# Performance work log

Measured on AMD Instinct MI355X. Metric: run time of the kernel, lower is better.

Reference implementation:

```python
import jax, jax.numpy as jnp
import numpy as np

IN_FEATURES = 8192
OUT_FEATURES = 8192
NNZ = 671088  # in*out*(1-0.99)
BATCH = 1024


def setup_inputs() -> dict:
    key = jax.random.key(0)
    kx, kv, kr, kc = jax.random.split(key, 4)
    x = jax.random.normal(kx, (BATCH, IN_FEATURES), dtype=jnp.float32)
    # values initialized ~ N(0,1) / sqrt(in_features), matching the module
    values = jax.random.normal(kv, (NNZ,), dtype=jnp.float32) * (1.0 / np.sqrt(IN_FEATURES))
    bias = jnp.zeros((OUT_FEATURES,), dtype=jnp.float32)
    rows = jax.random.randint(kr, (NNZ,), 0, IN_FEATURES, dtype=jnp.int32)
    cols = jax.random.randint(kc, (NNZ,), 0, OUT_FEATURES, dtype=jnp.int32)
    return {"x": x, "values": values, "bias": bias, "rows": rows, "cols": cols}


def reference(x, values, bias, rows, cols):
    # Materialize the sparse (in, out) weight via scatter-add.
    # Duplicate (row, col) pairs sum, matching torch COO .coalesce().
    W = jnp.zeros((IN_FEATURES, OUT_FEATURES), dtype=values.dtype)
    W = W.at[rows, cols].add(values)
    # res = addmm(bias, x, W) == x @ W + bias
    return x @ W + bias[None, :]
```

## Files before the change

### kernel.cpp

```cpp
#include <hip/hip_runtime.h>
#include <stdint.h>

#define IN_F   8192
#define OUT_F  8192
#define BATCH  1024
#define BT     8
#define NBT    (BATCH / BT)
#define MAIN_THREADS 1024
#define GROUPS_PER_WAVE 4
#define L_PREF 160
#define XTILE_BYTES (IN_F * 16)
#define CSTRIDE 16

#if __has_builtin(__builtin_amdgcn_fdot2) && __has_builtin(__builtin_amdgcn_perm)
#define USE_DOT2 1
typedef _Float16 half2v __attribute__((ext_vector_type(2)));
#else
#define USE_DOT2 0
#endif

typedef float f32x2 __attribute__((ext_vector_type(2)));


__device__ __forceinline__ unsigned f32_to_bf16_bits_rne(float f) {
    union { float f; unsigned u; } v; v.f = f;
    unsigned u = v.u;
    unsigned r = u + 0x7FFFu + ((u >> 16) & 1u);
    return r >> 16;
}
__device__ __forceinline__ float bf16_hi_bits_to_f32(unsigned b) {
    union { unsigned u; float f; } v; v.u = b & 0xFFFF0000u; return v.f;
}
__device__ __forceinline__ f32x2 unpack_pair(unsigned u) {
    union { unsigned u; float f; } lo, hi;
    lo.u = u << 16; hi.u = u & 0xFFFF0000u;
    f32x2 r; r.x = lo.f; r.y = hi.f; return r;
}

#if USE_DOT2
__device__ __forceinline__ unsigned val_bits(float f) {
    return (unsigned)__builtin_bit_cast(unsigned short, (_Float16)f);
}
__device__ __forceinline__ unsigned x_bits(float f) {
    return (unsigned)__builtin_bit_cast(unsigned short, (_Float16)f);
}
#else
__device__ __forceinline__ unsigned val_bits(float f) { return f32_to_bf16_bits_rne(f); }
__device__ __forceinline__ unsigned x_bits(float f)   { return f32_to_bf16_bits_rne(f); }
#endif

__global__ void scatter_kernel(const int* __restrict__ rows, const int* __restrict__ cols,
                               const float* __restrict__ vals,
                               int* __restrict__ counts, unsigned* __restrict__ ell,
                               int nnz, int L) {
    int t = blockIdx.x * blockDim.x + threadIdx.x;
    int i0 = t * 4;
    if (i0 + 3 < nnz) {
        int4   r4 = *(const int4*)(rows + i0);
        int4   c4 = *(const int4*)(cols + i0);
        float4 v4 = *(const float4*)(vals + i0);
        int c0 = c4.x, c1 = c4.y, c2 = c4.z, c3 = c4.w;
        unsigned pk0 = (val_bits(v4.x) << 16) | ((unsigned)r4.x << 3);
        unsigned pk1 = (val_bits(v4.y) << 16) | ((unsigned)r4.y << 3);
        unsigned pk2 = (val_bits(v4.z) << 16) | ((unsigned)r4.z << 3);
        unsigned pk3 = (val_bits(v4.w) << 16) | ((unsigned)r4.w << 3);
        int s0 = atomicAdd(&counts[c0 * CSTRIDE], 1);
        int s1 = atomicAdd(&counts[c1 * CSTRIDE], 1);
        int s2 = atomicAdd(&counts[c2 * CSTRIDE], 1);
        int s3 = atomicAdd(&counts[c3 * CSTRIDE], 1);
        if (s0 < L) ell[(size_t)(c0 >> 6) * (L * 64) + ((s0 >> 2) << 8) + ((c0 & 63) << 2) + (s0 & 3)] = pk0;
        if (s1 < L) ell[(size_t)(c1 >> 6) * (L * 64) + ((s1 >> 2) << 8) + ((c1 & 63) << 2) + (s1 & 3)] = pk1;
        if (s2 < L) ell[(size_t)(c2 >> 6) * (L * 64) + ((s2 >> 2) << 8) + ((c2 & 63) << 2) + (s2 & 3)] = pk2;
        if (s3 < L) ell[(size_t)(c3 >> 6) * (L * 64) + ((s3 >> 2) << 8) + ((c3 & 63) << 2) + (s3 & 3)] = pk3;
    } else {
        for (int i = i0; i < nnz; ++i) {
            int c = cols[i];
            unsigned pk = (val_bits(vals[i]) << 16) | ((unsigned)rows[i] << 3);
            int s = atomicAdd(&counts[c * CSTRIDE], 1);
            if (s < L)
                ell[(size_t)(c >> 6) * (L * 64) + ((s >> 2) << 8) + ((c & 63) << 2) + (s & 3)] = pk;
        }
    }
}

#if USE_DOT2
__device__ __forceinline__ void process_pair8(unsigned pk0, unsigned pk1, const char* xbase,
        float& a0, float& a1, float& a2, float& a3,
        float& a4, float& a5, float& a6, float& a7) {
    unsigned off0 = pk0 & 0xFFF8u;
    unsigned off1 = pk1 & 0xFFF8u;
    uint4 q0 = *(const uint4*)(xbase + off0 * 2);
    uint4 q1 = *(const uint4*)(xbase + off1 * 2);
    unsigned vv = __builtin_amdgcn_perm(pk1, pk0, 0x07060302u);
    half2v vh = __builtin_bit_cast(half2v, vv);
    unsigned e0 = __builtin_amdgcn_perm(q1.x, q0.x, 0x05040100u);
    unsigned o0 = __builtin_amdgcn_perm(q1.x, q0.x, 0x07060302u);
    unsigned e1 = __builtin_amdgcn_perm(q1.y, q0.y, 0x05040100u);
    unsigned o1 = __builtin_amdgcn_perm(q1.y, q0.y, 0x07060302u);
    unsigned e2 = __builtin_amdgcn_perm(q1.z, q0.z, 0x05040100u);
    unsigned o2 = __builtin_amdgcn_perm(q1.z, q0.z, 0x07060302u);
    unsigned e3 = __builtin_amdgcn_perm(q1.w, q0.w, 0x05040100u);
    unsigned o3 = __builtin_amdgcn_perm(q1.w, q0.w, 0x07060302u);
    a0 = __builtin_amdgcn_fdot2(__builtin_bit_cast(half2v, e0), vh, a0, false);
    a1 = __builtin_amdgcn_fdot2(__builtin_bit_cast(half2v, o0), vh, a1, false);
    a2 = __builtin_amdgcn_fdot2(__builtin_bit_cast(half2v, e1), vh, a2, false);
    a3 = __builtin_amdgcn_fdot2(__builtin_bit_cast(half2v, o1), vh, a3, false);
    a4 = __builtin_amdgcn_fdot2(__builtin_bit_cast(half2v, e2), vh, a4, false);
    a5 = __builtin_amdgcn_fdot2(__builtin_bit_cast(half2v, o2), vh, a5, false);
    a6 = __builtin_amdgcn_fdot2(__builtin_bit_cast(half2v, e3), vh, a6, false);
    a7 = __builtin_amdgcn_fdot2(__builtin_bit_cast(half2v, o3), vh, a7, false);
}
#else
__device__ __forceinline__ void process_entry8(unsigned pk, const char* xbase,
                                               f32x2& a01, f32x2& a23, f32x2& a45, f32x2& a67) {
    float val = bf16_hi_bits_to_f32(pk);
    f32x2 vv; vv.x = val; vv.y = val;
    unsigned off = pk & 0xFFF8u;
    uint4 d = *(const uint4*)(xbase + off * 2);
    a01 = __builtin_elementwise_fma(unpack_pair(d.x), vv, a01);
    a23 = __builtin_elementwise_fma(unpack_pair(d.y), vv, a23);
    a45 = __builtin_elementwise_fma(unpack_pair(d.z), vv, a45);
    a67 = __builtin_elementwise_fma(unpack_pair(d.w), vv, a67);
}
#endif

__global__ __launch_bounds__(MAIN_THREADS) void spmm_kernel(
        const float* __restrict__ x,
        const float* __restrict__ bias,
        const int* __restrict__ counts,
        const unsigned* __restrict__ ell,
        float* __restrict__ out, int L) {
    extern __shared__ uint4 xl[];
    int w = blockIdx.x;
    int bt = w >> 1;
    int half = w & 1;
    int t = threadIdx.x;
    int b0 = bt * BT;

    for (int r = t; r < IN_F; r += MAIN_THREADS) {
        unsigned u0 = x_bits(x[(b0 + 0) * IN_F + r]);
        unsigned u1 = x_bits(x[(b0 + 1) * IN_F + r]);
        unsigned u2 = x_bits(x[(b0 + 2) * IN_F + r]);
        unsigned u3 = x_bits(x[(b0 + 3) * IN_F + r]);
        unsigned u4 = x_bits(x[(b0 + 4) * IN_F + r]);
        unsigned u5 = x_bits(x[(b0 + 5) * IN_F + r]);
        unsigned u6 = x_bits(x[(b0 + 6) * IN_F + r]);
        unsigned u7 = x_bits(x[(b0 + 7) * IN_F + r]);
        uint4 d;
        d.x = (u1 << 16) | u0;
        d.y = (u3 << 16) | u2;
        d.z = (u5 << 16) | u4;
        d.w = (u7 << 16) | u6;
        xl[r] = d;
    }
    __syncthreads();

    const char* xbase = (const char*)xl;
    int wave = t >> 6;
    int lane = t & 63;
    int n4cap = L >> 2;

#pragma unroll 1
    for (int it = 0; it < GROUPS_PER_WAVE; ++it) {
        int g = half * 64 + wave * GROUPS_PER_WAVE + it;
        int col = (g << 6) + lane;
        int cnt = counts[col * CSTRIDE];
#pragma unroll
        for (int off = 32; off; off >>= 1) cnt = max(cnt, __shfl_xor(cnt, off, 64));
        int n4 = (cnt + 3) >> 2;
        n4 = min(n4, n4cap);
        const uint4* ep = (const uint4*)(ell + (size_t)g * (L * 64));
        float bv = bias[col];
#if USE_DOT2
        float a0 = 0.f, a1 = 0.f, a2 = 0.f, a3 = 0.f;
        float a4 = 0.f, a5 = 0.f, a6 = 0.f, a7 = 0.f;
        if (n4 > 0) {
            uint4 q = ep[lane];
#pragma unroll 1
            for (int s4 = 1; s4 < n4; ++s4) {
                uint4 qn = ep[s4 * 64 + lane];
                process_pair8(q.x, q.y, xbase, a0, a1, a2, a3, a4, a5, a6, a7);
                process_pair8(q.z, q.w, xbase, a0, a1, a2, a3, a4, a5, a6, a7);
                q = qn;
            }
            process_pair8(q.x, q.y, xbase, a0, a1, a2, a3, a4, a5, a6, a7);
            process_pair8(q.z, q.w, xbase, a0, a1, a2, a3, a4, a5, a6, a7);
        }
        out[(size_t)(b0 + 0) * OUT_F + col] = a0 + bv;
        out[(size_t)(b0 + 1) * OUT_F + col] = a1 + bv;
        out[(size_t)(b0 + 2) * OUT_F + col] = a2 + bv;
        out[(size_t)(b0 + 3) * OUT_F + col] = a3 + bv;
        out[(size_t)(b0 + 4) * OUT_F + col] = a4 + bv;
        out[(size_t)(b0 + 5) * OUT_F + col] = a5 + bv;
        out[(size_t)(b0 + 6) * OUT_F + col] = a6 + bv;
        out[(size_t)(b0 + 7) * OUT_F + col] = a7 + bv;
#else
        f32x2 a01 = {0.f, 0.f}, a23 = {0.f, 0.f}, a45 = {0.f, 0.f}, a67 = {0.f, 0.f};
        if (n4 > 0) {
            uint4 q = ep[lane];
#pragma unroll 1
            for (int s4 = 1; s4 < n4; ++s4) {
                uint4 qn = ep[s4 * 64 + lane];
                process_entry8(q.x, xbase, a01, a23, a45, a67);
                process_entry8(q.y, xbase, a01, a23, a45, a67);
                process_entry8(q.z, xbase, a01, a23, a45, a67);
                process_entry8(q.w, xbase, a01, a23, a45, a67);
                q = qn;
            }
            process_entry8(q.x, xbase, a01, a23, a45, a67);
            process_entry8(q.y, xbase, a01, a23, a45, a67);
            process_entry8(q.z, xbase, a01, a23, a45, a67);
            process_entry8(q.w, xbase, a01, a23, a45, a67);
        }
        out[(size_t)(b0 + 0) * OUT_F + col] = a01.x + bv;
        out[(size_t)(b0 + 1) * OUT_F + col] = a01.y + bv;
        out[(size_t)(b0 + 2) * OUT_F + col] = a23.x + bv;
        out[(size_t)(b0 + 3) * OUT_F + col] = a23.y + bv;
        out[(size_t)(b0 + 4) * OUT_F + col] = a45.x + bv;
        out[(size_t)(b0 + 5) * OUT_F + col] = a45.y + bv;
        out[(size_t)(b0 + 6) * OUT_F + col] = a67.x + bv;
        out[(size_t)(b0 + 7) * OUT_F + col] = a67.y + bv;
#endif
    }
}

extern "C" void kernel_launch(void* const* d_in, const int* in_sizes, int n_in,
                              void* d_out, int out_size, void* d_ws, size_t ws_size,
                              hipStream_t stream) {
    const float* x      = (const float*)d_in[0];
    const float* values = (const float*)d_in[1];
    const float* bias   = (const float*)d_in[2];
    const int* rows = (const int*)d_in[3];
    const int* cols = (const int*)d_in[4];
    float* out = (float*)d_out;
    int nnz = in_sizes[1];

    int* counts = (int*)d_ws;
    unsigned* ell = (unsigned*)counts + 8192 * CSTRIDE;

    long long cap_slots = ((long long)(ws_size / 4) - 8192LL * CSTRIDE) / 8192;
    int L = (int)(cap_slots & ~3LL);
    if (L > L_PREF) L = L_PREF;
    if (L < 4) L = 4;

    size_t zero_bytes = (size_t)(8192 * CSTRIDE + (size_t)L * 8192) * 4;

    static int attr_set = -1;
    if (attr_set < 0) {
        hipFuncSetAttribute((const void*)spmm_kernel,
                            hipFuncAttributeMaxDynamicSharedMemorySize, XTILE_BYTES);
        attr_set = 1;
    }

    hipMemsetAsync(d_ws, 0, zero_bytes, stream);
    int nthreads = (nnz + 3) / 4;
    scatter_kernel<<<(nthreads + 255) / 256, 256, 0, stream>>>(rows, cols, values,
                                                               counts, ell, nnz, L);
    spmm_kernel<<<NBT * 2, MAIN_THREADS, XTILE_BYTES, stream>>>(x, bias, counts, ell, out, L);
}
```

Measured before the change: 176.7 us.

## Replace global-atomic ELL scatter with two-pass bucketed binning and build

Replaces the per-nonzero global atomic scatter into the ELL layout with two passes. The first pass bins entries into 1024 buckets of 8 columns, using shared-memory counting, a prefix scan and one global atomic per bucket per block. The second pass sorts each 64-column group into ELL slots in shared memory and writes them out. This removes most global atomics and the large memset of the ELL buffer, since only the bucket counters are zeroed and the build pass writes padding explicitly. The cost is an extra kernel launch and an extra round trip through global memory for the staged entries.

```diff
diff --git a/kernel.cpp b/kernel.cpp
--- a/kernel.cpp
+++ b/kernel.cpp
@@ -10,7 +10,13 @@
 #define GROUPS_PER_WAVE 4
 #define L_PREF 160
 #define XTILE_BYTES (IN_F * 16)
-#define CSTRIDE 16
+
+#define NBUCKET 1024
+#define P1_THREADS 1024
+#define P1_PER 8
+#define P1_CHUNK (P1_THREADS * P1_PER)
+#define P2_THREADS 1024
+#define BIN_STRIDE (L_PREF + 1)
 
 #if __has_builtin(__builtin_amdgcn_fdot2) && __has_builtin(__builtin_amdgcn_perm)
 #define USE_DOT2 1
@@ -49,37 +55,132 @@
 __device__ __forceinline__ unsigned x_bits(float f)   { return f32_to_bf16_bits_rne(f); }
 #endif
 
-__global__ void scatter_kernel(const int* __restrict__ rows, const int* __restrict__ cols,
-                               const float* __restrict__ vals,
-                               int* __restrict__ counts, unsigned* __restrict__ ell,
-                               int nnz, int L) {
-    int t = blockIdx.x * blockDim.x + threadIdx.x;
-    int i0 = t * 4;
-    if (i0 + 3 < nnz) {
-        int4   r4 = *(const int4*)(rows + i0);
-        int4   c4 = *(const int4*)(cols + i0);
-        float4 v4 = *(const float4*)(vals + i0);
-        int c0 = c4.x, c1 = c4.y, c2 = c4.z, c3 = c4.w;
-        unsigned pk0 = (val_bits(v4.x) << 16) | ((unsigned)r4.x << 3);
-        unsigned pk1 = (val_bits(v4.y) << 16) | ((unsigned)r4.y << 3);
-        unsigned pk2 = (val_bits(v4.z) << 16) | ((unsigned)r4.z << 3);
-        unsigned pk3 = (val_bits(v4.w) << 16) | ((unsigned)r4.w << 3);
-        int s0 = atomicAdd(&counts[c0 * CSTRIDE], 1);
-        int s1 = atomicAdd(&counts[c1 * CSTRIDE], 1);
-        int s2 = atomicAdd(&counts[c2 * CSTRIDE], 1);
-        int s3 = atomicAdd(&counts[c3 * CSTRIDE], 1);
-        if (s0 < L) ell[(size_t)(c0 >> 6) * (L * 64) + ((s0 >> 2) << 8) + ((c0 & 63) << 2) + (s0 & 3)] = pk0;
-        if (s1 < L) ell[(size_t)(c1 >> 6) * (L * 64) + ((s1 >> 2) << 8) + ((c1 & 63) << 2) + (s1 & 3)] = pk1;
-        if (s2 < L) ell[(size_t)(c2 >> 6) * (L * 64) + ((s2 >> 2) << 8) + ((c2 & 63) << 2) + (s2 & 3)] = pk2;
-        if (s3 < L) ell[(size_t)(c3 >> 6) * (L * 64) + ((s3 >> 2) << 8) + ((c3 & 63) << 2) + (s3 & 3)] = pk3;
-    } else {
-        for (int i = i0; i < nnz; ++i) {
+__global__ __launch_bounds__(P1_THREADS) void bin_kernel(
+        const int* __restrict__ rows, const int* __restrict__ cols,
+        const float* __restrict__ vals,
+        int* __restrict__ bcnt, unsigned* __restrict__ ell, int nnz, int L) {
+    __shared__ int lcnt[NBUCKET];
+    __shared__ int lbase[NBUCKET];
+    __shared__ int gbase[NBUCKET];
+    __shared__ int wsum[16];
+    __shared__ unsigned stage[P1_CHUNK];
+    __shared__ unsigned short smap[P1_CHUNK];
+
+    int tid = threadIdx.x;
+    int i0 = blockIdx.x * P1_CHUNK;
+    lcnt[tid] = 0;
+    __syncthreads();
+
+    unsigned mypk[P1_PER];
+    int      myb[P1_PER];
+    int      myrk[P1_PER];
+#pragma unroll
+    for (int k = 0; k < P1_PER; ++k) {
+        int i = i0 + k * P1_THREADS + tid;
+        myb[k] = -1;
+        mypk[k] = 0;
+        myrk[k] = 0;
+        if (i < nnz) {
             int c = cols[i];
-            unsigned pk = (val_bits(vals[i]) << 16) | ((unsigned)rows[i] << 3);
-            int s = atomicAdd(&counts[c * CSTRIDE], 1);
-            if (s < L)
-                ell[(size_t)(c >> 6) * (L * 64) + ((s >> 2) << 8) + ((c & 63) << 2) + (s & 3)] = pk;
-        }
+            mypk[k] = (val_bits(vals[i]) << 16) | ((unsigned)rows[i] << 3) | ((unsigned)c & 7u);
+            myb[k] = c >> 3;
+            myrk[k] = atomicAdd(&lcnt[c >> 3], 1);
+        }
+    }
+    __syncthreads();
+
+    {
+        int wv = tid >> 6, ln = tid & 63;
+        int v = lcnt[tid];
+        int sc = v;
+#pragma unroll
+        for (int off = 1; off < 64; off <<= 1) {
+            int o = __shfl_up(sc, off, 64);
+            if (ln >= off) sc += o;
+        }
+        if (ln == 63) wsum[wv] = sc;
+        __syncthreads();
+        if (tid < 16) {
+            int s = wsum[tid];
+            int sl = s;
+#pragma unroll
+            for (int off = 1; off < 16; off <<= 1) {
+                int o = __shfl_up(sl, off, 16);
+                if (tid >= off) sl += o;
+            }
+            wsum[tid] = sl - s;
+        }
+        __syncthreads();
+        lbase[tid] = sc - v + wsum[wv];
+    }
+    __syncthreads();
+
+    {
+        int lc = lcnt[tid];
+        gbase[tid] = lc ? atomicAdd(&bcnt[tid], lc) : 0;
+    }
+#pragma unroll
+    for (int k = 0; k < P1_PER; ++k) {
+        if (myb[k] >= 0) {
+            int pos = lbase[myb[k]] + myrk[k];
+            stage[pos] = mypk[k];
+            smap[pos] = (unsigned short)myb[k];
+        }
+    }
+    __syncthreads();
+
+    int total = lbase[NBUCKET - 1] + lcnt[NBUCKET - 1];
+    int cap = 8 * L;
+    for (int i = tid; i < total; i += P1_THREADS) {
+        int b = smap[i];
+        int idx = gbase[b] + (i - lbase[b]);
+        if (idx < cap)
+            ell[(size_t)b * cap + idx] = stage[i];
+    }
+}
+
+__global__ __launch_bounds__(P2_THREADS) void build_kernel(
+        const int* __restrict__ bcnt, unsigned* __restrict__ ell,
+        int* __restrict__ counts, int L) {
+    __shared__ unsigned bins[64 * BIN_STRIDE];
+    __shared__ int ccnt[64];
+    __shared__ int qsh;
+    int g = blockIdx.x;
+    int tid = threadIdx.x;
+    for (int i = tid; i < 64 * BIN_STRIDE; i += P2_THREADS) bins[i] = 0;
+    if (tid < 64) ccnt[tid] = 0;
+    __syncthreads();
+
+    unsigned* slab = ell + (size_t)g * (64 * L);
+    int cap = 8 * L;
+#pragma unroll 1
+    for (int q = 0; q < 8; ++q) {
+        int cb = bcnt[g * 8 + q];
+        if (cb > cap) cb = cap;
+        const unsigned* bp = slab + q * cap;
+        for (int i = tid; i < cb; i += P2_THREADS) {
+            unsigned e = bp[i];
+            int c64 = q * 8 + (int)(e & 7u);
+            int rk = atomicAdd(&ccnt[c64], 1);
+            if (rk < L) bins[c64 * BIN_STRIDE + rk] = e;
+        }
+    }
+    __syncthreads();
+
+    if (tid < 64) {
+        int c = ccnt[tid];
+        counts[g * 64 + tid] = c;
+        int mc = min(c, L);
+#pragma unroll
+        for (int off = 32; off; off >>= 1) mc = max(mc, __shfl_xor(mc, off, 64));
+        if (tid == 0) qsh = (mc + 3) >> 2;
+    }
+    __syncthreads();
+
+    int D = qsh << 8;
+    for (int d = tid; d < D; d += P2_THREADS) {
+        int q = d >> 8, r = d & 255;
+        slab[d] = bins[(r >> 2) * BIN_STRIDE + q * 4 + (r & 3)];
     }
 }
 
@@ -164,7 +265,7 @@
     for (int it = 0; it < GROUPS_PER_WAVE; ++it) {
         int g = half * 64 + wave * GROUPS_PER_WAVE + it;
         int col = (g << 6) + lane;
-        int cnt = counts[col * CSTRIDE];
+        int cnt = counts[col];
 #pragma unroll
         for (int off = 32; off; off >>= 1) cnt = max(cnt, __shfl_xor(cnt, off, 64));
         int n4 = (cnt + 3) >> 2;
@@ -235,15 +336,14 @@
     float* out = (float*)d_out;
     int nnz = in_sizes[1];
 
-    int* counts = (int*)d_ws;
-    unsigned* ell = (unsigned*)counts + 8192 * CSTRIDE;
-
-    long long cap_slots = ((long long)(ws_size / 4) - 8192LL * CSTRIDE) / 8192;
+    int* bcnt   = (int*)d_ws;
+    int* counts = bcnt + NBUCKET;
+    unsigned* ell = (unsigned*)(counts + 8192);
+
+    long long cap_slots = ((long long)(ws_size / 4) - (NBUCKET + 8192)) / 8192;
     int L = (int)(cap_slots & ~3LL);
     if (L > L_PREF) L = L_PREF;
     if (L < 4) L = 4;
-
-    size_t zero_bytes = (size_t)(8192 * CSTRIDE + (size_t)L * 8192) * 4;
 
     static int attr_set = -1;
     if (attr_set < 0) {
@@ -252,9 +352,9 @@
         attr_set = 1;
     }
 
-    hipMemsetAsync(d_ws, 0, zero_bytes, stream);
-    int nthreads = (nnz + 3) / 4;
-    scatter_kernel<<<(nthreads + 255) / 256, 256, 0, stream>>>(rows, cols, values,
-                                                               counts, ell, nnz, L);
+    hipMemsetAsync(bcnt, 0, NBUCKET * 4, stream);
+    int nb1 = (nnz + P1_CHUNK - 1) / P1_CHUNK;
+    bin_kernel<<<nb1, P1_THREADS, 0, stream>>>(rows, cols, values, bcnt, ell, nnz, L);
+    build_kernel<<<128, P2_THREADS, 0, stream>>>(bcnt, ell, counts, L);
     spmm_kernel<<<NBT * 2, MAIN_THREADS, XTILE_BYTES, stream>>>(x, bias, counts, ell, out, L);
 }
```

After: 162.1 us. 1.09x faster.
